# Optimization experiments

Measured on AMD Instinct MI355X. Metric: run time of the kernel, lower is better.

## Reference

```python
import math
import jax, jax.numpy as jnp
import numpy as np

B, S, D, H, V, NZ = 2, 2048, 1024, 16, 4096, 10
DK = D // H
KAPPA = 1.0
GAMMA_VALS = [14.1347, 21.022, 25.0109, 30.4249, 32.9351,
              37.5862, 40.9187, 43.3271, 48.0052, 49.7738]


def setup_inputs() -> dict:
    key = jax.random.key(0)
    ks = jax.random.split(key, 12)
    w_scale = 1.0 / math.sqrt(D)
    x = jax.random.normal(ks[0], (B, S, D), dtype=jnp.float32)
    wq = jax.random.normal(ks[1], (D, D), dtype=jnp.float32) * w_scale
    wk = jax.random.normal(ks[2], (D, D), dtype=jnp.float32) * w_scale
    wv = jax.random.normal(ks[3], (D, D), dtype=jnp.float32) * w_scale
    wo = jax.random.normal(ks[4], (D, D), dtype=jnp.float32) * w_scale
    bq = jax.random.normal(ks[5], (D,), dtype=jnp.float32) * 0.01
    bk = jax.random.normal(ks[6], (D,), dtype=jnp.float32) * 0.01
    bv = jax.random.normal(ks[7], (D,), dtype=jnp.float32) * 0.01
    bo = jax.random.normal(ks[8], (D,), dtype=jnp.float32) * 0.01
    semantic_token_ids = jax.random.randint(ks[9], (B, S), 0, V)
    # constitutional charter mask: mostly-allowed boolean (stored as float buffer)
    omega_mask = (jax.random.uniform(ks[10], (V, V)) < 0.95).astype(jnp.float32)
    causal_mask = jnp.tril(jnp.ones((S, S), dtype=bool))
    gamma = jnp.asarray(GAMMA_VALS[:NZ], dtype=jnp.float32)
    return {
        "x": x, "wq": wq, "bq": bq, "wk": wk, "bk": bk,
        "wv": wv, "bv": bv, "wo": wo, "bo": bo,
        "omega_mask": omega_mask, "gamma": gamma,
        "semantic_token_ids": semantic_token_ids, "causal_mask": causal_mask,
    }


def _memory_kernel(seq_len, gamma):
    idx = jnp.arange(seq_len, dtype=jnp.float32)
    delta = jnp.abs(idx[:, None] - idx[None, :])            # [S, S]
    decay = jnp.exp(-KAPPA * delta)
    log_delta = jnp.log(delta + 1.0)
    cos_sum = jnp.sum(jnp.cos(gamma[:, None, None] * log_delta[None]), axis=0)
    return decay * cos_sum                                   # [S, S]


def reference(x, wq, bq, wk, bk, wv, bv, wo, bo,
              omega_mask, gamma, semantic_token_ids, causal_mask):
    batch, seq_len, _ = x.shape
    q = (x @ wq.T + bq).reshape(batch, seq_len, H, DK)
    k = (x @ wk.T + bk).reshape(batch, seq_len, H, DK)
    v = (x @ wv.T + bv).reshape(batch, seq_len, H, DK)
    scores = jnp.einsum('bihd,bjhd->bhij', q, k) / math.sqrt(DK)  # [B,H,S,S]
    M = _memory_kernel(seq_len, gamma)                            # [S,S]
    scores = scores * M[None, None]
    # seq_omega[b,i,j] = omega_mask[ids[b,i], ids[b,j]]
    ids = semantic_token_ids
    seq_omega = omega_mask[ids[:, :, None], ids[:, None, :]]      # [B,S,S]
    scores = jnp.where(seq_omega[:, None] == 0, -1e9, scores)
    scores = jnp.where(causal_mask[None, None], scores, -1e9)
    attn = jax.nn.softmax(scores, axis=-1)
    out = jnp.einsum('bhij,bjhd->bihd', attn, v).reshape(batch, seq_len, D)
    return out @ wo.T + bo
```

## Files before the change

### kernel.cpp

```cpp
#include <hip/hip_runtime.h>
#include <math.h>
#include <float.h>

#define B_ 2
#define S_ 2048
#define D_ 1024
#define H_ 16
#define V_ 4096
#define NZ_ 10
#define BS_ (B_ * S_)

typedef __attribute__((ext_vector_type(8))) __bf16 bf16x8;
typedef __attribute__((ext_vector_type(4))) float f32x4;

#define MFMA16(a, b, c) __builtin_amdgcn_mfma_f32_16x16x32_bf16((a), (b), (c), 0, 0, 0)

__device__ __forceinline__ unsigned short f2bf(float f) {
  unsigned u = __builtin_bit_cast(unsigned, f);
  u = (u + 0x7FFFu + ((u >> 16) & 1u)) >> 16;
  return (unsigned short)u;
}
__device__ __forceinline__ float bf2f(unsigned short h) {
  unsigned u = ((unsigned)h) << 16;
  return __builtin_bit_cast(float, u);
}

template <bool WLO>
__global__ __launch_bounds__(256) void split_kernel(const float* __restrict__ in,
                                                    unsigned short* __restrict__ hi,
                                                    unsigned short* __restrict__ lo) {
  int i = (blockIdx.x * 256 + threadIdx.x) * 4;
  float4 x = *(const float4*)(in + i);
  ushort4 h;
  h.x = f2bf(x.x); h.y = f2bf(x.y); h.z = f2bf(x.z); h.w = f2bf(x.w);
  *(ushort4*)(hi + i) = h;
  if (WLO) {
    ushort4 l;
    l.x = f2bf(x.x - bf2f(h.x));
    l.y = f2bf(x.y - bf2f(h.y));
    l.z = f2bf(x.z - bf2f(h.z));
    l.w = f2bf(x.w - bf2f(h.w));
    *(ushort4*)(lo + i) = l;
  }
}

__global__ __launch_bounds__(256) void split_w4_kernel(
    const float* __restrict__ wq, const float* __restrict__ wk,
    const float* __restrict__ wv, const float* __restrict__ wo,
    unsigned short* __restrict__ wqh, unsigned short* __restrict__ wql,
    unsigned short* __restrict__ wkh, unsigned short* __restrict__ wkl,
    unsigned short* __restrict__ wvh, unsigned short* __restrict__ woh) {
  int idx = (blockIdx.x * 256 + threadIdx.x) * 4;
  int w = idx >> 20;
  int off = idx & ((1 << 20) - 1);
  const float* src; unsigned short* hi; unsigned short* lo;
  if (w == 0)      { src = wq; hi = wqh; lo = wql; }
  else if (w == 1) { src = wk; hi = wkh; lo = wkl; }
  else if (w == 2) { src = wv; hi = wvh; lo = nullptr; }
  else             { src = wo; hi = woh; lo = nullptr; }
  float4 x = *(const float4*)(src + off);
  ushort4 h;
  h.x = f2bf(x.x); h.y = f2bf(x.y); h.z = f2bf(x.z); h.w = f2bf(x.w);
  *(ushort4*)(hi + off) = h;
  if (lo) {
    ushort4 l;
    l.x = f2bf(x.x - bf2f(h.x));
    l.y = f2bf(x.y - bf2f(h.y));
    l.z = f2bf(x.z - bf2f(h.z));
    l.w = f2bf(x.w - bf2f(h.w));
    *(ushort4*)(lo + off) = l;
  }
}

__global__ __launch_bounds__(256) void omega_pack_kernel(const float* __restrict__ omega,
                                                         unsigned long long* __restrict__ obit) {
  int e = blockIdx.x * 256 + threadIdx.x;
  bool ok = omega[e] != 0.f;
  unsigned long long mask = __ballot(ok);
  if ((threadIdx.x & 63) == 0) obit[e >> 6] = mask;
}

__global__ __launch_bounds__(256) void mfma_gemm_qkv(
    const unsigned short* __restrict__ xh, const unsigned short* __restrict__ xl,
    const unsigned short* __restrict__ wqh, const unsigned short* __restrict__ wql,
    const unsigned short* __restrict__ wkh, const unsigned short* __restrict__ wkl,
    const unsigned short* __restrict__ wvh,
    const float* __restrict__ bq, const float* __restrict__ bk,
    const float* __restrict__ bv,
    unsigned short* __restrict__ qoh, unsigned short* __restrict__ qol,
    unsigned short* __restrict__ koh, unsigned short* __restrict__ kol,
    unsigned short* __restrict__ voh) {
  __shared__ unsigned short tiles[4 * 4096];
  const int t = threadIdx.x;
  const int wave = t >> 6, lane = t & 63;
  const int which = blockIdx.x >> 3;
  const int n0 = (blockIdx.x & 7) * 128;
  const int i0 = blockIdx.y * 128;
  const int K = D_, N = D_;
  const int wm = wave >> 1, wn = wave & 1;
  const int m = lane & 15, quad = lane >> 4;

  const unsigned short* Wh = (which == 0) ? wqh : (which == 1) ? wkh : wvh;
  const unsigned short* Wl = (which == 0) ? wql : wkl;
  const float* bias = (which == 0) ? bq : (which == 1) ? bk : bv;
  unsigned short* Chi = (which == 0) ? qoh : (which == 1) ? koh : voh;
  unsigned short* Clo = (which == 0) ? qol : (which == 1) ? kol : nullptr;
  const bool split = (which < 2);
  const int ntiles = split ? 4 : 2;

  const unsigned short* gb[4];
  gb[0] = xh + (size_t)i0 * K;
  gb[1] = Wh + (size_t)n0 * K;
  gb[2] = xl + (size_t)i0 * K;
  gb[3] = Wl + (size_t)n0 * K;

  f32x4 acc[4][4] = {};

  for (int k0 = 0; k0 < K; k0 += 32) {
    __syncthreads();
    for (int cc = wave; cc < ntiles * 8; cc += 4) {
      int tile = cc >> 3, c = cc & 7;
      int s = (c << 6) + lane;
      int row = s >> 2;
      int cq = (s & 3) ^ ((s >> 3) & 3);
      const unsigned short* g = gb[tile] + (size_t)row * K + k0 + (cq << 3);
      unsigned short* l = &tiles[tile * 4096 + (s << 3)];
      __builtin_amdgcn_global_load_lds((const __attribute__((address_space(1))) void*)g,
                                       (__attribute__((address_space(3))) void*)l,
                                       16, 0, 0);
    }
    __syncthreads();

    bf16x8 afh[4], bfh[4];
#pragma unroll
    for (int mt = 0; mt < 4; ++mt) {
      int r = wm * 64 + mt * 16 + m;
      afh[mt] = *(const bf16x8*)&tiles[0 * 4096 + r * 32 + ((quad ^ ((r >> 1) & 3)) << 3)];
    }
#pragma unroll
    for (int nt = 0; nt < 4; ++nt) {
      int r = wn * 64 + nt * 16 + m;
      bfh[nt] = *(const bf16x8*)&tiles[1 * 4096 + r * 32 + ((quad ^ ((r >> 1) & 3)) << 3)];
    }
    if (split) {
      bf16x8 afl[4], bfl[4];
#pragma unroll
      for (int mt = 0; mt < 4; ++mt) {
        int r = wm * 64 + mt * 16 + m;
        afl[mt] = *(const bf16x8*)&tiles[2 * 4096 + r * 32 + ((quad ^ ((r >> 1) & 3)) << 3)];
      }
#pragma unroll
      for (int nt = 0; nt < 4; ++nt) {
        int r = wn * 64 + nt * 16 + m;
        bfl[nt] = *(const bf16x8*)&tiles[3 * 4096 + r * 32 + ((quad ^ ((r >> 1) & 3)) << 3)];
      }
#pragma unroll
      for (int mt = 0; mt < 4; ++mt)
#pragma unroll
        for (int nt = 0; nt < 4; ++nt) {
          acc[mt][nt] = MFMA16(afh[mt], bfh[nt], acc[mt][nt]);
          acc[mt][nt] = MFMA16(afl[mt], bfh[nt], acc[mt][nt]);
          acc[mt][nt] = MFMA16(afh[mt], bfl[nt], acc[mt][nt]);
        }
    } else {
#pragma unroll
      for (int mt = 0; mt < 4; ++mt)
#pragma unroll
        for (int nt = 0; nt < 4; ++nt)
          acc[mt][nt] = MFMA16(afh[mt], bfh[nt], acc[mt][nt]);
    }
  }

  float bvv[4];
#pragma unroll
  for (int nt = 0; nt < 4; ++nt) bvv[nt] = bias[n0 + wn * 64 + nt * 16 + m];
#pragma unroll
  for (int mt = 0; mt < 4; ++mt) {
    int rbase = i0 + wm * 64 + mt * 16 + quad * 4;
#pragma unroll
    for (int nt = 0; nt < 4; ++nt) {
      int col = n0 + wn * 64 + nt * 16 + m;
#pragma unroll
      for (int r = 0; r < 4; ++r) {
        float val = acc[mt][nt][r] + bvv[nt];
        size_t idx = (size_t)(rbase + r) * N + col;
        unsigned short hv = f2bf(val);
        Chi[idx] = hv;
        if (Clo) Clo[idx] = f2bf(val - bf2f(hv));
      }
    }
  }
}

__global__ __launch_bounds__(256) void mfma_gemm_o(const unsigned short* __restrict__ Ah,
                                                   const unsigned short* __restrict__ Wh,
                                                   const float* __restrict__ bias,
                                                   float* __restrict__ C,
                                                   int M, int N, int K) {
  __shared__ unsigned short tiles[2 * 4096];
  const int t = threadIdx.x;
  const int wave = t >> 6, lane = t & 63;
  const int i0 = blockIdx.y * 128, n0 = blockIdx.x * 128;
  const int wm = wave >> 1, wn = wave & 1;
  const int m = lane & 15, quad = lane >> 4;

  const unsigned short* gb[2];
  gb[0] = Ah + (size_t)i0 * K;
  gb[1] = Wh + (size_t)n0 * K;

  f32x4 acc[4][4] = {};
  for (int k0 = 0; k0 < K; k0 += 32) {
    __syncthreads();
    for (int cc = wave; cc < 16; cc += 4) {
      int tile = cc >> 3, c = cc & 7;
      int s = (c << 6) + lane;
      int row = s >> 2;
      int cq = (s & 3) ^ ((s >> 3) & 3);
      const unsigned short* g = gb[tile] + (size_t)row * K + k0 + (cq << 3);
      unsigned short* l = &tiles[tile * 4096 + (s << 3)];
      __builtin_amdgcn_global_load_lds((const __attribute__((address_space(1))) void*)g,
                                       (__attribute__((address_space(3))) void*)l,
                                       16, 0, 0);
    }
    __syncthreads();
    bf16x8 afh[4], bfh[4];
#pragma unroll
    for (int mt = 0; mt < 4; ++mt) {
      int r = wm * 64 + mt * 16 + m;
      afh[mt] = *(const bf16x8*)&tiles[0 * 4096 + r * 32 + ((quad ^ ((r >> 1) & 3)) << 3)];
    }
#pragma unroll
    for (int nt = 0; nt < 4; ++nt) {
      int r = wn * 64 + nt * 16 + m;
      bfh[nt] = *(const bf16x8*)&tiles[1 * 4096 + r * 32 + ((quad ^ ((r >> 1) & 3)) << 3)];
    }
#pragma unroll
    for (int mt = 0; mt < 4; ++mt)
#pragma unroll
      for (int nt = 0; nt < 4; ++nt)
        acc[mt][nt] = MFMA16(afh[mt], bfh[nt], acc[mt][nt]);
  }

  float bvv[4];
#pragma unroll
  for (int nt = 0; nt < 4; ++nt) bvv[nt] = bias[n0 + wn * 64 + nt * 16 + m];
#pragma unroll
  for (int mt = 0; mt < 4; ++mt) {
    int rbase = i0 + wm * 64 + mt * 16 + quad * 4;
#pragma unroll
    for (int nt = 0; nt < 4; ++nt) {
      int col = n0 + wn * 64 + nt * 16 + m;
#pragma unroll
      for (int r = 0; r < 4; ++r)
        C[(size_t)(rbase + r) * N + col] = acc[mt][nt][r] + bvv[nt];
    }
  }
}

__global__ void ts8_kernel(const unsigned short* __restrict__ vh, float* __restrict__ ts8) {
  int idx = blockIdx.x * 256 + threadIdx.x;
  int d = idx % D_;
  int bg = idx / D_;
  int g = bg % 256;
  int b = bg / 256;
  const unsigned short* p = vh + (size_t)(b * S_ + g * 8) * D_ + d;
  float s = 0.f;
#pragma unroll
  for (int j = 0; j < 8; ++j) s += bf2f(p[(size_t)j * D_]);
  ts8[idx] = s;
}

__global__ void ts64_kernel(const float* __restrict__ ts8, float* __restrict__ ts64) {
  int idx = blockIdx.x * 256 + threadIdx.x;
  int d = idx % D_;
  int bT = idx / D_;
  int T = bT % 32;
  int b = bT / 32;
  float s = 0.f;
#pragma unroll
  for (int u = 0; u < 8; ++u) s += ts8[((size_t)b * 256 + T * 8 + u) * D_ + d];
  ts64[idx] = s;
}

__global__ void tsp2_kernel(const float* __restrict__ ts64, float* __restrict__ tsp) {
  int idx = blockIdx.x * 256 + threadIdx.x;
  int d = idx % D_;
  int bT = idx / D_;
  int T = bT % 33;
  int b = bT / 33;
  float s = 0.f;
  for (int u = 0; u < T; ++u) s += ts64[((size_t)b * 32 + u) * D_ + d];
  tsp[idx] = s;
}

__global__ __launch_bounds__(256) void bandmask_kernel(const int* __restrict__ ids,
                                                       const unsigned long long* __restrict__ obit,
                                                       unsigned long long* __restrict__ bm) {
  int row = blockIdx.x * 4 + (threadIdx.x >> 6);
  int lane = threadIdx.x & 63;
  int b = row / S_, i = row % S_;
  int idi = ids[row];
  int j = i - lane;
  bool ok = false;
  if (j >= 0) {
    int idj = ids[b * S_ + j];
    ok = (obit[((size_t)idi << 6) + (idj >> 6)] >> (idj & 63)) & 1ull;
  }
  unsigned long long mask = __ballot(ok);
  if (lane == 0) bm[row] = mask;
}

__global__ __launch_bounds__(256) void farsum_kernel(const unsigned short* __restrict__ vh,
                                                     const float* __restrict__ ts8,
                                                     const float* __restrict__ tsp,
                                                     const int* __restrict__ ids,
                                                     const unsigned long long* __restrict__ obit,
                                                     unsigned short* __restrict__ farsum,
                                                     int* __restrict__ c0) {
  const int b = blockIdx.x / S_;
  const int i = blockIdx.x % S_;
  const int t = threadIdx.x;
  if (i < 64) {
    if (t == 0) c0[blockIdx.x] = 0;
    return;
  }
  const int jmax = i - 64;
  const int F = jmax + 1;
  const int d0 = t * 4;
  const int T = F >> 6;
  const int G8 = (F & 63) >> 3;

  float4 acc = *(const float4*)(tsp + ((size_t)b * 33 + T) * D_ + d0);
  for (int u = 0; u < G8; ++u) {
    float4 x = *(const float4*)(ts8 + ((size_t)b * 256 + T * 8 + u) * D_ + d0);
    acc.x += x.x; acc.y += x.y; acc.z += x.z; acc.w += x.w;
  }
  for (int j = (T << 6) + (G8 << 3); j <= jmax; ++j) {
    ushort4 x = *(const ushort4*)(vh + ((size_t)(b * S_) + j) * D_ + d0);
    acc.x += bf2f(x.x); acc.y += bf2f(x.y);
    acc.z += bf2f(x.z); acc.w += bf2f(x.w);
  }

  __shared__ int list[256];
  __shared__ int cnt;
  const int idi = ids[b * S_ + i];
  const unsigned long long* orow = obit + ((size_t)idi << 6);
  int nmask = 0;
  for (int base = 0; base < F; base += 256) {
    if (t == 0) cnt = 0;
    __syncthreads();
    int j = base + t;
    if (j <= jmax) {
      int idj = ids[b * S_ + j];
      if (!((orow[idj >> 6] >> (idj & 63)) & 1ull)) list[atomicAdd(&cnt, 1)] = j;
    }
    __syncthreads();
    int c = cnt;
    nmask += c;
    for (int mm = 0; mm < c; ++mm) {
      int jm = list[mm];
      ushort4 x = *(const ushort4*)(vh + ((size_t)(b * S_) + jm) * D_ + d0);
      acc.x -= bf2f(x.x); acc.y -= bf2f(x.y);
      acc.z -= bf2f(x.z); acc.w -= bf2f(x.w);
    }
    __syncthreads();
  }
  ushort4 o;
  o.x = f2bf(acc.x); o.y = f2bf(acc.y); o.z = f2bf(acc.z); o.w = f2bf(acc.w);
  *(ushort4*)(farsum + (size_t)(b * S_ + i) * D_ + d0) = o;
  if (t == 0) c0[blockIdx.x] = F - nmask;
}

__global__ __launch_bounds__(256) void attn3_kernel(
    const unsigned short* __restrict__ qh, const unsigned short* __restrict__ ql,
    const unsigned short* __restrict__ kh, const unsigned short* __restrict__ kl,
    const unsigned short* __restrict__ vh, const unsigned short* __restrict__ farsum,
    const int* __restrict__ c0arr, const float* __restrict__ tsp,
    const unsigned long long* __restrict__ bm, const float* __restrict__ gamma,
    unsigned short* __restrict__ out) {
  const int h = blockIdx.x, i0 = blockIdx.y * 64, b = blockIdx.z;
  __shared__ unsigned short Qhs[64][72], Qls[64][72], Khs[64][72], KlP[64][72], Vt[64][72];
  __shared__ float mrow[64], lrow[64], arow[64], Mband[64];
  __shared__ float rmaxw[4][32], rsumw[4][32];
  __shared__ unsigned long long bmr[64];
  __shared__ int c0r[64];
  const int t = threadIdx.x, lane = t & 63, wave = t >> 6;
  const int m = lane & 15, quad = lane >> 4;
  const int wm = wave >> 1, wn = wave & 1;

  for (int c = t; c < 1024; c += 256) {
    int r = c >> 4, d4 = (c & 15) << 2;
    size_t g = ((size_t)(b * S_) + i0 + r) * D_ + h * 64 + d4;
    *(ushort4*)&Qhs[r][d4] = *(const ushort4*)(qh + g);
    *(ushort4*)&Qls[r][d4] = *(const ushort4*)(ql + g);
  }
  if (t < 64) {
    float delta = (float)t;
    float ld = logf(delta + 1.f);
    float cs = 0.f;
#pragma unroll
    for (int z = 0; z < NZ_; ++z) cs += cosf(gamma[z] * ld);
    Mband[t] = expf(-delta) * cs * 0.125f;
    int grow = b * S_ + i0 + t;
    bmr[t] = bm[grow];
    int c0v = c0arr[grow];
    c0r[t] = c0v;
    mrow[t] = (c0v > 0) ? 0.f : -FLT_MAX;
    lrow[t] = 0.f;
  }
  f32x4 accO[2][2] = {};

  for (int pass = 0; pass < 2; ++pass) {
    const int jt0 = i0 + (pass - 1) * 64;
    if (jt0 < 0) continue;
    __syncthreads();
    for (int c = t; c < 1024; c += 256) {
      int r = c >> 4, d4 = (c & 15) << 2;
      size_t g = ((size_t)(b * S_) + jt0 + r) * D_ + h * 64 + d4;
      *(ushort4*)&Khs[r][d4] = *(const ushort4*)(kh + g);
      *(ushort4*)&KlP[r][d4] = *(const ushort4*)(kl + g);
      ushort4 vv = *(const ushort4*)(vh + g);
      Vt[d4 + 0][r] = vv.x; Vt[d4 + 1][r] = vv.y;
      Vt[d4 + 2][r] = vv.z; Vt[d4 + 3][r] = vv.w;
    }
    __syncthreads();
    f32x4 accS[2][2] = {};
#pragma unroll
    for (int kc = 0; kc < 2; ++kc) {
      bf16x8 aH[2], aL[2], bH[2], bL[2];
#pragma unroll
      for (int mt = 0; mt < 2; ++mt) {
        aH[mt] = *(const bf16x8*)&Qhs[wm * 32 + mt * 16 + m][kc * 32 + quad * 8];
        aL[mt] = *(const bf16x8*)&Qls[wm * 32 + mt * 16 + m][kc * 32 + quad * 8];
      }
#pragma unroll
      for (int nt = 0; nt < 2; ++nt) {
        bH[nt] = *(const bf16x8*)&Khs[wn * 32 + nt * 16 + m][kc * 32 + quad * 8];
        bL[nt] = *(const bf16x8*)&KlP[wn * 32 + nt * 16 + m][kc * 32 + quad * 8];
      }
#pragma unroll
      for (int mt = 0; mt < 2; ++mt)
#pragma unroll
        for (int nt = 0; nt < 2; ++nt) {
          accS[mt][nt] = MFMA16(aH[mt], bH[nt], accS[mt][nt]);
          accS[mt][nt] = MFMA16(aL[mt], bH[nt], accS[mt][nt]);
          accS[mt][nt] = MFMA16(aH[mt], bL[nt], accS[mt][nt]);
        }
    }
    float rmx[2][4];
#pragma unroll
    for (int mt = 0; mt < 2; ++mt)
#pragma unroll
      for (int r = 0; r < 4; ++r) rmx[mt][r] = -FLT_MAX;
#pragma unroll
    for (int mt = 0; mt < 2; ++mt)
#pragma unroll
      for (int nt = 0; nt < 2; ++nt)
#pragma unroll
        for (int r = 0; r < 4; ++r) {
          int il = wm * 32 + mt * 16 + quad * 4 + r;
          int jl = wn * 32 + nt * 16 + m;
          int dlt = (pass == 0) ? (il + 64 - jl) : (il - jl);
          float s = -FLT_MAX;
          if (dlt >= 0 && dlt < 64 && ((bmr[il] >> dlt) & 1ull))
            s = accS[mt][nt][r] * Mband[dlt];
          accS[mt][nt][r] = s;
          rmx[mt][r] = fmaxf(rmx[mt][r], s);
        }
#pragma unroll
    for (int off = 1; off < 16; off <<= 1)
#pragma unroll
      for (int mt = 0; mt < 2; ++mt)
#pragma unroll
        for (int r = 0; r < 4; ++r)
          rmx[mt][r] = fmaxf(rmx[mt][r], __shfl_xor(rmx[mt][r], off));
    if (m == 0)
#pragma unroll
      for (int mt = 0; mt < 2; ++mt)
#pragma unroll
        for (int r = 0; r < 4; ++r)
          rmaxw[wave][mt * 16 + quad * 4 + r] = rmx[mt][r];
    __syncthreads();
    if (t < 64) {
      int wmw = t >> 5, idx = t & 31;
      float tmax = fmaxf(rmaxw[wmw * 2][idx], rmaxw[wmw * 2 + 1][idx]);
      float mold = mrow[t], mnew = fmaxf(mold, tmax);
      arow[t] = expf(mold - mnew);
      mrow[t] = mnew;
    }
    __syncthreads();
    float rs[2][4] = {};
#pragma unroll
    for (int mt = 0; mt < 2; ++mt)
#pragma unroll
      for (int nt = 0; nt < 2; ++nt)
#pragma unroll
        for (int r = 0; r < 4; ++r) {
          int il = wm * 32 + mt * 16 + quad * 4 + r;
          int jl = wn * 32 + nt * 16 + m;
          float s = accS[mt][nt][r];
          float p = (s > -1e37f) ? expf(s - mrow[il]) : 0.f;
          rs[mt][r] += p;
          KlP[il][jl] = f2bf(p);
        }
#pragma unroll
    for (int off = 1; off < 16; off <<= 1)
#pragma unroll
      for (int mt = 0; mt < 2; ++mt)
#pragma unroll
        for (int r = 0; r < 4; ++r)
          rs[mt][r] += __shfl_xor(rs[mt][r], off);
    if (m == 0)
#pragma unroll
      for (int mt = 0; mt < 2; ++mt)
#pragma unroll
        for (int r = 0; r < 4; ++r)
          rsumw[wave][mt * 16 + quad * 4 + r] = rs[mt][r];
#pragma unroll
    for (int mt = 0; mt < 2; ++mt)
#pragma unroll
      for (int r = 0; r < 4; ++r) {
        float al = arow[wm * 32 + mt * 16 + quad * 4 + r];
        accO[mt][0][r] *= al;
        accO[mt][1][r] *= al;
      }
    __syncthreads();
    if (t < 64) {
      int wmw = t >> 5, idx = t & 31;
      lrow[t] = lrow[t] * arow[t] + rsumw[wmw * 2][idx] + rsumw[wmw * 2 + 1][idx];
    }
#pragma unroll
    for (int kc = 0; kc < 2; ++kc) {
      bf16x8 aP[2], bV[2];
#pragma unroll
      for (int mt = 0; mt < 2; ++mt)
        aP[mt] = *(const bf16x8*)&KlP[wm * 32 + mt * 16 + m][kc * 32 + quad * 8];
#pragma unroll
      for (int nt = 0; nt < 2; ++nt)
        bV[nt] = *(const bf16x8*)&Vt[wn * 32 + nt * 16 + m][kc * 32 + quad * 8];
#pragma unroll
      for (int mt = 0; mt < 2; ++mt)
#pragma unroll
        for (int nt = 0; nt < 2; ++nt)
          accO[mt][nt] = MFMA16(aP[mt], bV[nt], accO[mt][nt]);
    }
  }
  __syncthreads();
#pragma unroll
  for (int mt = 0; mt < 2; ++mt)
#pragma unroll
    for (int r = 0; r < 4; ++r) {
      int il = wm * 32 + mt * 16 + quad * 4 + r;
      int gi = i0 + il;
      float mv = mrow[il], l = lrow[il];
      int C0 = c0r[il];
      float efar = (C0 > 0) ? expf(-mv) : 0.f;
      float denom = l + (float)C0 * efar;
      bool degen = (l == 0.f && C0 == 0);
      if (degen) denom = (float)S_;
      float inv = 1.f / denom;
#pragma unroll
      for (int nt = 0; nt < 2; ++nt) {
        int d = wn * 32 + nt * 16 + m;
        size_t base = ((size_t)(b * S_) + gi) * D_ + h * 64 + d;
        float o = accO[mt][nt][r];
        if (C0 > 0) o += efar * bf2f(farsum[base]);
        if (degen) o = tsp[((size_t)b * 33 + 32) * D_ + h * 64 + d];
        out[base] = f2bf(o * inv);
      }
    }
}

extern "C" void kernel_launch(void* const* d_in, const int* in_sizes, int n_in,
                              void* d_out, int out_size, void* d_ws, size_t ws_size,
                              hipStream_t stream) {
  const float* x     = (const float*)d_in[0];
  const float* wq    = (const float*)d_in[1];
  const float* bq    = (const float*)d_in[2];
  const float* wk    = (const float*)d_in[3];
  const float* bk    = (const float*)d_in[4];
  const float* wv    = (const float*)d_in[5];
  const float* bv    = (const float*)d_in[6];
  const float* wo    = (const float*)d_in[7];
  const float* bo    = (const float*)d_in[8];
  const float* omega = (const float*)d_in[9];
  const float* gamma = (const float*)d_in[10];
  const int*   ids   = (const int*)d_in[11];
  float* out = (float*)d_out;

  char* ws = (char*)d_ws;
  const size_t SZH = (size_t)BS_ * D_ * 2;
  const size_t WH  = (size_t)D_ * D_ * 2;
  unsigned short* qhb = (unsigned short*)(ws);
  unsigned short* qlb = (unsigned short*)(ws + 1 * SZH);
  unsigned short* khb = (unsigned short*)(ws + 2 * SZH);
  unsigned short* klb = (unsigned short*)(ws + 3 * SZH);
  unsigned short* vhb = (unsigned short*)(ws + 4 * SZH);
  unsigned short* xl    = (unsigned short*)(ws + 5 * SZH);
  unsigned short* fsumh = xl;
  unsigned short* xh    = (unsigned short*)(ws + 6 * SZH);
  unsigned short* ah    = xh;
  char* wp = ws + 7 * SZH;
  unsigned short* wqh = (unsigned short*)(wp);
  unsigned short* wql = (unsigned short*)(wp + 1 * WH);
  unsigned short* wkh = (unsigned short*)(wp + 2 * WH);
  unsigned short* wkl = (unsigned short*)(wp + 3 * WH);
  unsigned short* wvh = (unsigned short*)(wp + 4 * WH);
  unsigned short* woh = (unsigned short*)(wp + 5 * WH);
  char* tail = wp + 6 * WH;
  unsigned long long* obit = (unsigned long long*)tail;
  float* ts8  = (float*)(tail + (size_t)V_ * 64 * 8);
  float* ts64 = (float*)((char*)ts8 + (size_t)B_ * 256 * D_ * 4);
  float* tsp  = (float*)((char*)ts64 + (size_t)B_ * 32 * D_ * 4);
  int* c0 = (int*)((char*)tsp + (size_t)B_ * 33 * D_ * 4);
  unsigned long long* bmask = (unsigned long long*)((char*)c0 + (size_t)BS_ * 4);

  split_kernel<true><<<(BS_ * D_) / 1024, 256, 0, stream>>>(x, xh, xl);
  omega_pack_kernel<<<(V_ * V_) / 256, 256, 0, stream>>>(omega, obit);
  split_w4_kernel<<<(4 * D_ * D_) / 1024, 256, 0, stream>>>(wq, wk, wv, wo,
                                                            wqh, wql, wkh, wkl, wvh, woh);

  mfma_gemm_qkv<<<dim3(24, 32), 256, 0, stream>>>(xh, xl, wqh, wql, wkh, wkl, wvh,
                                                  bq, bk, bv, qhb, qlb, khb, klb, vhb);

  ts8_kernel<<<(B_ * 256 * D_) / 256, 256, 0, stream>>>(vhb, ts8);
  ts64_kernel<<<(B_ * 32 * D_) / 256, 256, 0, stream>>>(ts8, ts64);
  tsp2_kernel<<<(B_ * 33 * D_) / 256, 256, 0, stream>>>(ts64, tsp);
  bandmask_kernel<<<(B_ * S_) / 4, 256, 0, stream>>>(ids, obit, bmask);
  farsum_kernel<<<B_ * S_, 256, 0, stream>>>(vhb, ts8, tsp, ids, obit, fsumh, c0);
  attn3_kernel<<<dim3(H_, S_ / 64, B_), 256, 0, stream>>>(qhb, qlb, khb, klb, vhb, fsumh, c0,
                                                          tsp, bmask, gamma, ah);

  mfma_gemm_o<<<dim3(D_ / 128, BS_ / 128), 256, 0, stream>>>(ah, woh, bo, out, BS_, D_, D_);
}
```

Measured before the change: 427.8 us.

## Double-buffer LDS tiles in QKV and output projection GEMMs

```diff
diff --git a/kernel.cpp b/kernel.cpp
--- a/kernel.cpp
+++ b/kernel.cpp
@@ -80,6 +80,63 @@
   if ((threadIdx.x & 63) == 0) obit[e >> 6] = mask;
 }
 
+template <int NT>
+__device__ __forceinline__ void stage_tiles(const unsigned short* const* gb,
+                                            int wave, int lane, int K, int k0,
+                                            unsigned short* dst) {
+#pragma unroll
+  for (int tile = 0; tile < NT; ++tile) {
+#pragma unroll
+    for (int half = 0; half < 2; ++half) {
+      int c = wave + half * 4;
+      int s = (c << 6) + lane;
+      int row = s >> 2;
+      int cq = (s & 3) ^ ((s >> 3) & 3);
+      const unsigned short* g = gb[tile] + (size_t)row * K + k0 + (cq << 3);
+      unsigned short* l = dst + tile * 4096 + (s << 3);
+      __builtin_amdgcn_global_load_lds((const __attribute__((address_space(1))) void*)g,
+                                       (__attribute__((address_space(3))) void*)l,
+                                       16, 0, 0);
+    }
+  }
+}
+
+__device__ __forceinline__ void frag_loads(const unsigned short* tb, int base, int wsel,
+                                           int m, int quad, bf16x8 (&f)[4]) {
+#pragma unroll
+  for (int i = 0; i < 4; ++i) {
+    int r = wsel * 64 + i * 16 + m;
+    f[i] = *(const bf16x8*)&tb[base + r * 32 + ((quad ^ ((r >> 1) & 3)) << 3)];
+  }
+}
+
+__device__ __forceinline__ void qkv_compute(const unsigned short* tb, bool split,
+                                            int wm, int wn, int m, int quad,
+                                            f32x4 (&acc)[4][4]) {
+  bf16x8 afh[4], bfh[4];
+  frag_loads(tb, 0 * 4096, wm, m, quad, afh);
+  frag_loads(tb, 1 * 4096, wn, m, quad, bfh);
+  if (split) {
+    bf16x8 afl[4], bfl[4];
+    frag_loads(tb, 2 * 4096, wm, m, quad, afl);
+    frag_loads(tb, 3 * 4096, wn, m, quad, bfl);
+#pragma unroll
+    for (int mt = 0; mt < 4; ++mt)
+#pragma unroll
+      for (int nt = 0; nt < 4; ++nt) {
+        acc[mt][nt] = MFMA16(afh[mt], bfh[nt], acc[mt][nt]);
+        acc[mt][nt] = MFMA16(afl[mt], bfh[nt], acc[mt][nt]);
+        acc[mt][nt] = MFMA16(afh[mt], bfl[nt], acc[mt][nt]);
+      }
+  } else {
+#pragma unroll
+    for (int mt = 0; mt < 4; ++mt)
+#pragma unroll
+      for (int nt = 0; nt < 4; ++nt)
+        acc[mt][nt] = MFMA16(afh[mt], bfh[nt], acc[mt][nt]);
+  }
+}
+
 __global__ __launch_bounds__(256) void mfma_gemm_qkv(
     const unsigned short* __restrict__ xh, const unsigned short* __restrict__ xl,
     const unsigned short* __restrict__ wqh, const unsigned short* __restrict__ wql,
@@ -90,7 +147,7 @@
     unsigned short* __restrict__ qoh, unsigned short* __restrict__ qol,
     unsigned short* __restrict__ koh, unsigned short* __restrict__ kol,
     unsigned short* __restrict__ voh) {
-  __shared__ unsigned short tiles[4 * 4096];
+  __shared__ unsigned short tiles[2][4 * 4096];
   const int t = threadIdx.x;
   const int wave = t >> 6, lane = t & 63;
   const int which = blockIdx.x >> 3;
@@ -106,7 +163,6 @@
   unsigned short* Chi = (which == 0) ? qoh : (which == 1) ? koh : voh;
   unsigned short* Clo = (which == 0) ? qol : (which == 1) ? kol : nullptr;
   const bool split = (which < 2);
-  const int ntiles = split ? 4 : 2;
 
   const unsigned short* gb[4];
   gb[0] = xh + (size_t)i0 * K;
@@ -116,59 +172,21 @@
 
   f32x4 acc[4][4] = {};
 
-  for (int k0 = 0; k0 < K; k0 += 32) {
-    __syncthreads();
-    for (int cc = wave; cc < ntiles * 8; cc += 4) {
-      int tile = cc >> 3, c = cc & 7;
-      int s = (c << 6) + lane;
-      int row = s >> 2;
-      int cq = (s & 3) ^ ((s >> 3) & 3);
-      const unsigned short* g = gb[tile] + (size_t)row * K + k0 + (cq << 3);
-      unsigned short* l = &tiles[tile * 4096 + (s << 3)];
-      __builtin_amdgcn_global_load_lds((const __attribute__((address_space(1))) void*)g,
-                                       (__attribute__((address_space(3))) void*)l,
-                                       16, 0, 0);
-    }
-    __syncthreads();
-
-    bf16x8 afh[4], bfh[4];
-#pragma unroll
-    for (int mt = 0; mt < 4; ++mt) {
-      int r = wm * 64 + mt * 16 + m;
-      afh[mt] = *(const bf16x8*)&tiles[0 * 4096 + r * 32 + ((quad ^ ((r >> 1) & 3)) << 3)];
-    }
-#pragma unroll
-    for (int nt = 0; nt < 4; ++nt) {
-      int r = wn * 64 + nt * 16 + m;
-      bfh[nt] = *(const bf16x8*)&tiles[1 * 4096 + r * 32 + ((quad ^ ((r >> 1) & 3)) << 3)];
-    }
-    if (split) {
-      bf16x8 afl[4], bfl[4];
-#pragma unroll
-      for (int mt = 0; mt < 4; ++mt) {
-        int r = wm * 64 + mt * 16 + m;
-        afl[mt] = *(const bf16x8*)&tiles[2 * 4096 + r * 32 + ((quad ^ ((r >> 1) & 3)) << 3)];
-      }
-#pragma unroll
-      for (int nt = 0; nt < 4; ++nt) {
-        int r = wn * 64 + nt * 16 + m;
-        bfl[nt] = *(const bf16x8*)&tiles[3 * 4096 + r * 32 + ((quad ^ ((r >> 1) & 3)) << 3)];
-      }
-#pragma unroll
-      for (int mt = 0; mt < 4; ++mt)
-#pragma unroll
-        for (int nt = 0; nt < 4; ++nt) {
-          acc[mt][nt] = MFMA16(afh[mt], bfh[nt], acc[mt][nt]);
-          acc[mt][nt] = MFMA16(afl[mt], bfh[nt], acc[mt][nt]);
-          acc[mt][nt] = MFMA16(afh[mt], bfl[nt], acc[mt][nt]);
-        }
-    } else {
-#pragma unroll
-      for (int mt = 0; mt < 4; ++mt)
-#pragma unroll
-        for (int nt = 0; nt < 4; ++nt)
-          acc[mt][nt] = MFMA16(afh[mt], bfh[nt], acc[mt][nt]);
-    }
+  if (split) stage_tiles<4>(gb, wave, lane, K, 0, tiles[0]);
+  else       stage_tiles<2>(gb, wave, lane, K, 0, tiles[0]);
+  __syncthreads();
+
+  for (int k0 = 0; k0 < K; k0 += 64) {
+    if (split) stage_tiles<4>(gb, wave, lane, K, k0 + 32, tiles[1]);
+    else       stage_tiles<2>(gb, wave, lane, K, k0 + 32, tiles[1]);
+    qkv_compute(tiles[0], split, wm, wn, m, quad, acc);
+    __syncthreads();
+    if (k0 + 64 < K) {
+      if (split) stage_tiles<4>(gb, wave, lane, K, k0 + 64, tiles[0]);
+      else       stage_tiles<2>(gb, wave, lane, K, k0 + 64, tiles[0]);
+    }
+    qkv_compute(tiles[1], split, wm, wn, m, quad, acc);
+    __syncthreads();
   }
 
   float bvv[4];
@@ -197,7 +215,7 @@
                                                    const float* __restrict__ bias,
                                                    float* __restrict__ C,
                                                    int M, int N, int K) {
-  __shared__ unsigned short tiles[2 * 4096];
+  __shared__ unsigned short tiles[2][2 * 4096];
   const int t = threadIdx.x;
   const int wave = t >> 6, lane = t & 63;
   const int i0 = blockIdx.y * 128, n0 = blockIdx.x * 128;
@@ -209,36 +227,17 @@
   gb[1] = Wh + (size_t)n0 * K;
 
   f32x4 acc[4][4] = {};
-  for (int k0 = 0; k0 < K; k0 += 32) {
-    __syncthreads();
-    for (int cc = wave; cc < 16; cc += 4) {
-      int tile = cc >> 3, c = cc & 7;
-      int s = (c << 6) + lane;
-      int row = s >> 2;
-      int cq = (s & 3) ^ ((s >> 3) & 3);
-      const unsigned short* g = gb[tile] + (size_t)row * K + k0 + (cq << 3);
-      unsigned short* l = &tiles[tile * 4096 + (s << 3)];
-      __builtin_amdgcn_global_load_lds((const __attribute__((address_space(1))) void*)g,
-                                       (__attribute__((address_space(3))) void*)l,
-                                       16, 0, 0);
-    }
-    __syncthreads();
-    bf16x8 afh[4], bfh[4];
-#pragma unroll
-    for (int mt = 0; mt < 4; ++mt) {
-      int r = wm * 64 + mt * 16 + m;
-      afh[mt] = *(const bf16x8*)&tiles[0 * 4096 + r * 32 + ((quad ^ ((r >> 1) & 3)) << 3)];
-    }
-#pragma unroll
-    for (int nt = 0; nt < 4; ++nt) {
-      int r = wn * 64 + nt * 16 + m;
-      bfh[nt] = *(const bf16x8*)&tiles[1 * 4096 + r * 32 + ((quad ^ ((r >> 1) & 3)) << 3)];
-    }
-#pragma unroll
-    for (int mt = 0; mt < 4; ++mt)
-#pragma unroll
-      for (int nt = 0; nt < 4; ++nt)
-        acc[mt][nt] = MFMA16(afh[mt], bfh[nt], acc[mt][nt]);
+
+  stage_tiles<2>(gb, wave, lane, K, 0, tiles[0]);
+  __syncthreads();
+
+  for (int k0 = 0; k0 < K; k0 += 64) {
+    stage_tiles<2>(gb, wave, lane, K, k0 + 32, tiles[1]);
+    qkv_compute(tiles[0], false, wm, wn, m, quad, acc);
+    __syncthreads();
+    if (k0 + 64 < K) stage_tiles<2>(gb, wave, lane, K, k0 + 64, tiles[0]);
+    qkv_compute(tiles[1], false, wm, wn, m, quad, acc);
+    __syncthreads();
   }
 
   float bvv[4];
```

Result: faster. 385.6 us (-9.9%).
